# Performance work log

Hardware: AMD Instinct MI355X
Metric: run time of the kernel (lower is better)

The kernel has to match this reference:

```python
import jax, jax.numpy as jnp
import numpy as np

H = 16        # num heads
ALPHA = 1.3   # entmax alpha
N_ITER = 50   # bisection iterations
EPS = 1e-5    # layernorm eps


def entmax_bisect(x, alpha=ALPHA, n_iter=N_ITER):
    # x: (..., K). Bisection entmax along last axis (Peters et al. 2019).
    am1 = alpha - 1.0
    x = x - jnp.max(x, axis=-1, keepdims=True)
    m = jnp.max(x, axis=-1, keepdims=True)  # == 0 after shift
    lo, hi = m - 10.0, m + 10.0
    def step(carry, _):
        lo, hi = carry
        mid = 0.5 * (lo + hi)
        p = jnp.maximum(am1 * x - mid, 0.0) ** (1.0 / am1)
        gt = jnp.sum(p, axis=-1, keepdims=True) > 1.0
        return (jnp.where(gt, mid, lo), jnp.where(gt, hi, mid)), None
    (lo, hi), _ = jax.lax.scan(jax.checkpoint(step), (lo, hi), None, length=n_iter)
    p = jnp.maximum(am1 * x - hi, 0.0) ** (1.0 / am1)
    return p / (jnp.sum(p, axis=-1, keepdims=True) + 1e-12)


def _heads(t, B, N, hd):
    return t.reshape(B, N, H, hd).transpose(0, 2, 1, 3)  # (B,H,N,hd)


def attn_branch(x, mask, wq, bq, wk, bk, wv, bv, wo, bo, use_entmax):
    B, N, D = x.shape
    hd = D // H
    q = _heads(x @ wq + bq, B, N, hd)
    k = _heads(x @ wk + bk, B, N, hd)
    v = _heads(x @ wv + bv, B, N, hd)
    s = jnp.einsum('bhqd,bhkd->bhqk', q, k) / float(np.sqrt(hd)) + mask
    if use_entmax:
        s = s - jnp.max(s, axis=-1, keepdims=True)
        a = entmax_bisect(s)
    else:
        a = jax.nn.softmax(s, axis=-1)
    o = jnp.einsum('bhqk,bhkd->bhqd', a, v).transpose(0, 2, 1, 3).reshape(B, N, D)
    return o @ wo + bo


def layer_norm(x, g, b):
    m = jnp.mean(x, axis=-1, keepdims=True)
    v = jnp.mean((x - m) ** 2, axis=-1, keepdims=True)
    return (x - m) * jax.lax.rsqrt(v + EPS) * g + b


def setup_inputs():
    B, N, D, F, FILM, NMODS = 4, 512, 2048, 8192, 64, 10000
    key = jax.random.key(0)
    ks = iter(jax.random.split(key, 64))
    rn = lambda *s: jax.random.normal(next(ks), s, dtype=jnp.float32)
    inp = dict(
        x=rn(B, N, D),
        attn_mask_intra=jnp.zeros((N, N), jnp.float32),
        attn_mask_inter=jnp.zeros((N, N), jnp.float32),
        mods=jax.random.randint(next(ks), (B, N), 0, 9999),
        film_emb=rn(NMODS, FILM) * 0.02,
        film_gw=rn(FILM, D) * 0.02, film_gb=jnp.zeros((D,), jnp.float32),
        film_bw=rn(FILM, D) * 0.02, film_bb=jnp.zeros((D,), jnp.float32),
        gate_alpha=jnp.zeros((2,), jnp.float32),
        ln1_g=jnp.ones((D,), jnp.float32), ln1_b=jnp.zeros((D,), jnp.float32),
        ln2_g=jnp.ones((D,), jnp.float32), ln2_b=jnp.zeros((D,), jnp.float32),
        ffn_w1=rn(D, F) * 0.02, ffn_b1=jnp.zeros((F,), jnp.float32),
        ffn_w2=rn(F, D) * 0.02, ffn_b2=jnp.zeros((D,), jnp.float32),
    )
    for tag in ('a', 'e'):
        for nm in ('q', 'k', 'v', 'o'):
            inp['w%s_%s' % (nm, tag)] = rn(D, D) * 0.02
            inp['b%s_%s' % (nm, tag)] = jnp.zeros((D,), jnp.float32)
    return inp


def reference(x, attn_mask_intra, attn_mask_inter, mods,
              film_emb, film_gw, film_gb, film_bw, film_bb,
              gate_alpha, ln1_g, ln1_b, ln2_g, ln2_b,
              ffn_w1, ffn_b1, ffn_w2, ffn_b2,
              wq_a, bq_a, wk_a, bk_a, wv_a, bv_a, wo_a, bo_a,
              wq_e, bq_e, wk_e, bk_e, wv_e, bv_e, wo_e, bo_e):
    # FiLM modulation on the intra-module branch input
    e = film_emb[jnp.clip(mods, 1, None)]                      # (B,N,FILM)
    y_intra = (1.0 + e @ film_gw + film_gb) * x + (e @ film_bw + film_bb)
    z_intra = attn_branch(y_intra, attn_mask_intra, wq_a, bq_a, wk_a, bk_a,
                          wv_a, bv_a, wo_a, bo_a, use_entmax=False)
    z_inter = attn_branch(x, attn_mask_inter, wq_e, bq_e, wk_e, bk_e,
                          wv_e, bv_e, wo_e, bo_e, use_entmax=True)
    w = jax.nn.softmax(gate_alpha)                              # global gate
    z = w[0] * z_intra + w[1] * z_inter
    h = layer_norm(x + z, ln1_g, ln1_b)                         # Post-LN
    y = jax.nn.relu(h @ ffn_w1 + ffn_b1) @ ffn_w2 + ffn_b2
    return layer_norm(h + y, ln2_g, ln2_b)
```

## Files before the change

kernel.cpp:

```cpp
#include <hip/hip_runtime.h>
#include <hip/hip_bf16.h>

typedef float f32x4 __attribute__((ext_vector_type(4)));
typedef short bf16x8 __attribute__((ext_vector_type(8)));
typedef unsigned short u16;

#define SEQ    512
#define DIM    2048
#define NHEAD  16
#define HDIM   128
#define BATCH  4
#define BTOK   2048
#define FFDIM  8192
#define DSZ    ((long)BTOK*DIM)
#define QKVN   (3*DIM)
#define QKVSZ  ((long)BTOK*QKVN)
#define ISS    0.08838834764831845f

__device__ __forceinline__ u16 f2bf(float f){
  union{float fv;unsigned u;}c;c.fv=f;
  unsigned r=c.u+0x7FFFu+((c.u>>16)&1u); return (u16)(r>>16);
}
__device__ __forceinline__ float bf2f(u16 v){
  union{unsigned u;float f;}c;c.u=((unsigned)v)<<16;return c.f;
}
__device__ __forceinline__ float pow103(float t){
  return __builtin_amdgcn_exp2f(__builtin_amdgcn_logf(t)*(10.0f/3.0f));
}

#define GLD16(g,l) __builtin_amdgcn_global_load_lds( \
    (const __attribute__((address_space(1))) unsigned int*)(g), \
    (__attribute__((address_space(3))) unsigned int*)(l), 16, 0, 0)

#define MF(a,b,c) __builtin_amdgcn_mfma_f32_16x16x32_bf16(a,b,c,0,0,0)
#define VMW(n) do{ asm volatile("s_waitcnt vmcnt(" #n ")" ::: "memory"); \
                   __builtin_amdgcn_sched_barrier(0); }while(0)
#define LGKM0() do{ asm volatile("s_waitcnt lgkmcnt(0)" ::: "memory"); \
                    __builtin_amdgcn_sched_barrier(0); }while(0)
#define BARR() do{ asm volatile("" ::: "memory"); __builtin_amdgcn_s_barrier(); \
                   asm volatile("" ::: "memory"); }while(0)

__global__ __launch_bounds__(256, 3)
void gemm4(const u16* __restrict__ A, int lda, long sAo, long sAi,
           const u16* __restrict__ B, int ldb, long sBo, long sBi,
           void* __restrict__ C, int ldc, long sCo, int outbf,
           const float* __restrict__ bias, long sbias,
           int K, int hdiv, int relu)
{
  __shared__ __align__(16) u16 sm[24576];
  char* smb = (char*)sm;

  int gx = gridDim.x, gy = gridDim.y;
  int nwg = gx*gy*gridDim.z;
  int flat = (blockIdx.z*gy + blockIdx.y)*gx + blockIdx.x;
  int cpx = nwg >> 3; flat = (flat & 7)*cpx + (flat >> 3);
  int by = flat % gy; int tq = flat / gy; int bx = tq % gx; int bz = tq / gx;

  int zo = bz / hdiv, zi = bz - zo*hdiv;
  const u16* Ab = A + (long)zo*sAo + (long)zi*sAi;
  const u16* Bb = B + (long)zo*sBo + (long)zi*sBi;
  int m0 = by*128, n0 = bx*128;

  int tid = threadIdx.x, lane = tid & 63, w = tid >> 6;
  int wrow = (w>>1)*64, wn = (w&1)*64;
  int lr = lane & 15, lg = lane >> 4;

  int stR[2], stC[2], ldsch[2];
  #pragma unroll
  for (int q = 0; q < 2; q++) {
    int chunk = q*4 + w;
    int r = chunk*16 + (lane>>2);
    int c = (lane&3)*16;
    int Rz = r ^ ((r>>2)&1);
    int Cz = c ^ ((((r>>2)^r)&1)<<4) ^ (((r>>1)&1)<<5);
    stR[q] = Rz; stC[q] = Cz>>1;
    ldsch[q] = chunk*1024;
  }

  int aoff = ((wrow + lr)*64 + lg*16) ^ ((lane&7)<<4);
  int boff = ((wn  + lr)*64 + lg*16) ^ ((lane&7)<<4);

  f32x4 acc[4][4] = {};
  int NT = K >> 5;

  auto STG = [&](int buf, int op, int kt) {
    const u16* gp = op ? Bb : Ab;
    int ld   = op ? ldb : lda;
    int base = op ? n0 : m0;
    int kcol = kt*32;
    #pragma unroll
    for (int q = 0; q < 2; q++) {
      const u16* src = gp + (long)(base + stR[q])*ld + kcol + stC[q];
      char* dst = smb + buf*16384 + op*8192 + ldsch[q];
      GLD16(src, dst);
    }
  };

  STG(0,0,0); STG(0,1,0);
  STG(1,0,1); STG(1,1,1);

  int buf = 0;
  for (int t = 0; t < NT; t++) {
    char* Ax = smb + buf*16384;
    char* Bx = smb + buf*16384 + 8192;

    if (t+2 < NT) {
      int nb = buf + 2; if (nb >= 3) nb -= 3;
      STG(nb,0,t+2); STG(nb,1,t+2);
      VMW(8);
    } else if (t+1 < NT) { VMW(4); }
    else                 { VMW(0); }
    BARR();

    bf16x8 af[4], bv[4];
    #pragma unroll
    for (int i = 0; i < 4; i++) af[i] = *(const bf16x8*)(Ax + aoff + i*1024);
    #pragma unroll
    for (int j = 0; j < 4; j++) bv[j] = *(const bf16x8*)(Bx + boff + j*1024);
    LGKM0();
    __builtin_amdgcn_s_setprio(1);
    #pragma unroll
    for (int i = 0; i < 4; i++) {
      acc[i][0] = MF(af[i], bv[0], acc[i][0]);
      acc[i][1] = MF(af[i], bv[1], acc[i][1]);
      acc[i][2] = MF(af[i], bv[2], acc[i][2]);
      acc[i][3] = MF(af[i], bv[3], acc[i][3]);
    }
    __builtin_amdgcn_s_setprio(0);
    BARR();
    buf++; if (buf == 3) buf = 0;
  }

  if (outbf) {
    u16* Cb = (u16*)C + (long)bz*sCo;
    #pragma unroll
    for (int j = 0; j < 4; j++) {
      int col = n0 + wn + j*16 + lr;
      float bv2 = bias ? bias[zo*sbias + col] : 0.0f;
      #pragma unroll
      for (int i = 0; i < 4; i++) {
        #pragma unroll
        for (int e = 0; e < 4; e++) {
          int row = m0 + wrow + i*16 + lg*4 + e;
          float v = acc[i][j][e] + bv2;
          if (relu) v = fmaxf(v, 0.0f);
          Cb[(long)row*ldc + col] = f2bf(v);
        }
      }
    }
  } else {
    float* Cb = (float*)C + (long)bz*sCo;
    #pragma unroll
    for (int j = 0; j < 4; j++) {
      int col = n0 + wn + j*16 + lr;
      #pragma unroll
      for (int i = 0; i < 4; i++) {
        #pragma unroll
        for (int e = 0; e < 4; e++) {
          int row = m0 + wrow + i*16 + lg*4 + e;
          Cb[(long)row*ldc + col] = acc[i][j][e];
        }
      }
    }
  }
}

template<int ENTMAX>
__global__ __launch_bounds__(256, 2)
void qkprobs(const u16* __restrict__ QKVp, long brOff,
             const float* __restrict__ maskp, u16* __restrict__ P)
{
  __shared__ __align__(16) u16 sm[40960];
  char* smb = (char*)sm;

  int m0 = blockIdx.x*64;
  int z  = blockIdx.y;
  int b  = z >> 4, h = z & 15;
  const u16* Qb = QKVp + brOff + (long)b*SEQ*QKVN + h*HDIM;
  const u16* Kb = Qb + DIM;

  int tid = threadIdx.x, lane = tid & 63, w = tid >> 6;
  int lr = lane & 15, lg = lane >> 4;
  int wn = w*128;

  int rl = lane >> 2;
  int cb = (lane & 3)*16;

  int aoff = (lr*64 + lg*16) ^ ((lane&7)<<4);
  int boff = ((wn + lr)*64 + lg*16) ^ ((lane&7)<<4);

  auto stgA = [&](int kt) {
    int r = w*16 + rl;
    int Rz = r ^ ((r>>2)&1);
    int Cz = cb ^ ((((r>>2)^r)&1)<<4) ^ (((r>>1)&1)<<5);
    GLD16(Qb + (long)(m0+Rz)*QKVN + kt*32 + (Cz>>1), smb + kt*4096 + w*1024);
  };
  auto stgB = [&](int buf, int kt) {
    #pragma unroll
    for (int q = 0; q < 8; q++) {
      int chunk = q*4 + w;
      int r = chunk*16 + rl;
      int Rz = r ^ ((r>>2)&1);
      int Cz = cb ^ ((((r>>2)^r)&1)<<4) ^ (((r>>1)&1)<<5);
      GLD16(Kb + (long)Rz*QKVN + kt*32 + (Cz>>1),
            smb + 16384 + buf*32768 + chunk*1024);
    }
  };

  f32x4 acc[4][8] = {};

  stgA(0); stgA(1); stgA(2); stgA(3);
  stgB(0,0);

  #pragma unroll
  for (int kt = 0; kt < 4; kt++) {
    if (kt < 3) { stgB((kt+1)&1, kt+1); VMW(8); } else { VMW(0); }
    BARR();
    char* Bx = smb + 16384 + (kt&1)*32768;
    bf16x8 af[4], bv[8];
    #pragma unroll
    for (int i = 0; i < 4; i++) af[i] = *(const bf16x8*)(smb + kt*4096 + aoff + i*1024);
    #pragma unroll
    for (int j = 0; j < 8; j++) bv[j] = *(const bf16x8*)(Bx + boff + j*1024);
    LGKM0();
    __builtin_amdgcn_s_setprio(1);
    #pragma unroll
    for (int i = 0; i < 4; i++)
      #pragma unroll
      for (int j = 0; j < 8; j++)
        acc[i][j] = MF(af[i], bv[j], acc[i][j]);
    __builtin_amdgcn_s_setprio(0);
    BARR();
  }

  float* redA = (float*)smb;
  float* redB = (float*)(smb + 1024);

  float rmax[16];
  #pragma unroll
  for (int s = 0; s < 16; s++) rmax[s] = -3.4e38f;
  #pragma unroll
  for (int i = 0; i < 4; i++) {
    #pragma unroll
    for (int e = 0; e < 4; e++) {
      int row = i*16 + lg*4 + e;
      const float* mp = maskp + (long)(m0+row)*SEQ + wn + lr;
      #pragma unroll
      for (int j = 0; j < 8; j++) {
        float v = acc[i][j][e]*ISS + mp[j*16];
        acc[i][j][e] = v;
        rmax[i*4+e] = fmaxf(rmax[i*4+e], v);
      }
    }
  }
  #pragma unroll
  for (int s = 0; s < 16; s++)
    #pragma unroll
    for (int o = 1; o < 16; o <<= 1) rmax[s] = fmaxf(rmax[s], __shfl_xor(rmax[s], o));
  if (lr == 0) {
    #pragma unroll
    for (int i = 0; i < 4; i++)
      #pragma unroll
      for (int e = 0; e < 4; e++) redA[w*64 + i*16 + lg*4 + e] = rmax[i*4+e];
  }
  BARR();
  #pragma unroll
  for (int i = 0; i < 4; i++)
    #pragma unroll
    for (int e = 0; e < 4; e++) {
      int row = i*16 + lg*4 + e;
      rmax[i*4+e] = fmaxf(fmaxf(redA[row], redA[64+row]),
                          fmaxf(redA[128+row], redA[192+row]));
    }
  BARR();

  float inv[16];

  if (ENTMAX) {
    #pragma unroll
    for (int i = 0; i < 4; i++)
      #pragma unroll
      for (int j = 0; j < 8; j++)
        #pragma unroll
        for (int e = 0; e < 4; e++)
          acc[i][j][e] = (acc[i][j][e] - rmax[i*4+e])*0.3f;

    float lo[16], hi[16], tau[16];
    #pragma unroll
    for (int s = 0; s < 16; s++) { lo[s] = -1.0f; hi[s] = 0.0f; }

    #pragma unroll 1
    for (int it = 0; it < 5; it++) {
      float ps[16];
      #pragma unroll
      for (int s = 0; s < 16; s++) ps[s] = 0.0f;
      #pragma unroll
      for (int i = 0; i < 4; i++)
        #pragma unroll
        for (int e = 0; e < 4; e++) {
          float mid = 0.5f*(lo[i*4+e] + hi[i*4+e]);
          #pragma unroll
          for (int j = 0; j < 8; j++) {
            float t = acc[i][j][e] - mid;
            if (t > 0.0f) ps[i*4+e] += pow103(t);
          }
        }
      #pragma unroll
      for (int s = 0; s < 16; s++)
        #pragma unroll
        for (int o = 1; o < 16; o <<= 1) ps[s] += __shfl_xor(ps[s], o);
      if (lr == 0) {
        #pragma unroll
        for (int i = 0; i < 4; i++)
          #pragma unroll
          for (int e = 0; e < 4; e++) redA[w*64 + i*16 + lg*4 + e] = ps[i*4+e];
      }
      BARR();
      #pragma unroll
      for (int i = 0; i < 4; i++)
        #pragma unroll
        for (int e = 0; e < 4; e++) {
          int row = i*16 + lg*4 + e, s = i*4+e;
          float tot = redA[row] + redA[64+row] + redA[128+row] + redA[192+row];
          float mid = 0.5f*(lo[s] + hi[s]);
          bool gt = tot > 1.0f;
          lo[s] = gt ? mid : lo[s];
          hi[s] = gt ? hi[s] : mid;
        }
      BARR();
    }
    #pragma unroll
    for (int s = 0; s < 16; s++) tau[s] = 0.5f*(lo[s] + hi[s]);

    #pragma unroll 1
    for (int it = 0; it < 5; it++) {
      float ps[16], pd[16];
      #pragma unroll
      for (int s = 0; s < 16; s++) { ps[s] = 0.0f; pd[s] = 0.0f; }
      #pragma unroll
      for (int i = 0; i < 4; i++)
        #pragma unroll
        for (int e = 0; e < 4; e++) {
          float tv = tau[i*4+e];
          #pragma unroll
          for (int j = 0; j < 8; j++) {
            float t = acc[i][j][e] - tv;
            if (t > 0.0f) {
              float w7 = __builtin_amdgcn_exp2f(__builtin_amdgcn_logf(t)*(7.0f/3.0f));
              pd[i*4+e] += w7; ps[i*4+e] += w7*t;
            }
          }
        }
      #pragma unroll
      for (int s = 0; s < 16; s++)
        #pragma unroll
        for (int o = 1; o < 16; o <<= 1) {
          ps[s] += __shfl_xor(ps[s], o);
          pd[s] += __shfl_xor(pd[s], o);
        }
      if (lr == 0) {
        #pragma unroll
        for (int i = 0; i < 4; i++)
          #pragma unroll
          for (int e = 0; e < 4; e++) {
            redA[w*64 + i*16 + lg*4 + e] = ps[i*4+e];
            redB[w*64 + i*16 + lg*4 + e] = pd[i*4+e];
          }
      }
      BARR();
      #pragma unroll
      for (int i = 0; i < 4; i++)
        #pragma unroll
        for (int e = 0; e < 4; e++) {
          int row = i*16 + lg*4 + e, s = i*4+e;
          float st = redA[row] + redA[64+row] + redA[128+row] + redA[192+row];
          float dt = redB[row] + redB[64+row] + redB[128+row] + redB[192+row];
          bool gt = st > 1.0f;
          lo[s] = gt ? tau[s] : lo[s];
          hi[s] = gt ? hi[s] : tau[s];
          float tn = tau[s] + (st - 1.0f) / ((10.0f/3.0f)*dt + 1e-30f);
          tau[s] = (tn > lo[s] && tn < hi[s]) ? tn : 0.5f*(lo[s] + hi[s]);
        }
      BARR();
    }

    float ps[16];
    #pragma unroll
    for (int s = 0; s < 16; s++) ps[s] = 0.0f;
    #pragma unroll
    for (int i = 0; i < 4; i++)
      #pragma unroll
      for (int e = 0; e < 4; e++) {
        float tv = tau[i*4+e];
        #pragma unroll
        for (int j = 0; j < 8; j++) {
          float t = acc[i][j][e] - tv;
          float p = (t > 0.0f) ? pow103(t) : 0.0f;
          acc[i][j][e] = p;
          ps[i*4+e] += p;
        }
      }
    #pragma unroll
    for (int s = 0; s < 16; s++)
      #pragma unroll
      for (int o = 1; o < 16; o <<= 1) ps[s] += __shfl_xor(ps[s], o);
    if (lr == 0) {
      #pragma unroll
      for (int i = 0; i < 4; i++)
        #pragma unroll
        for (int e = 0; e < 4; e++) redA[w*64 + i*16 + lg*4 + e] = ps[i*4+e];
    }
    BARR();
    #pragma unroll
    for (int i = 0; i < 4; i++)
      #pragma unroll
      for (int e = 0; e < 4; e++) {
        int row = i*16 + lg*4 + e;
        inv[i*4+e] = 1.0f/(redA[row] + redA[64+row] + redA[128+row] + redA[192+row] + 1e-12f);
      }
  } else {
    float ps[16];
    #pragma unroll
    for (int s = 0; s < 16; s++) ps[s] = 0.0f;
    #pragma unroll
    for (int i = 0; i < 4; i++)
      #pragma unroll
      for (int e = 0; e < 4; e++) {
        float mx = rmax[i*4+e];
        #pragma unroll
        for (int j = 0; j < 8; j++) {
          float p = __expf(acc[i][j][e] - mx);
          acc[i][j][e] = p;
          ps[i*4+e] += p;
        }
      }
    #pragma unroll
    for (int s = 0; s < 16; s++)
      #pragma unroll
      for (int o = 1; o < 16; o <<= 1) ps[s] += __shfl_xor(ps[s], o);
    if (lr == 0) {
      #pragma unroll
      for (int i = 0; i < 4; i++)
        #pragma unroll
        for (int e = 0; e < 4; e++) redA[w*64 + i*16 + lg*4 + e] = ps[i*4+e];
    }
    BARR();
    #pragma unroll
    for (int i = 0; i < 4; i++)
      #pragma unroll
      for (int e = 0; e < 4; e++) {
        int row = i*16 + lg*4 + e;
        inv[i*4+e] = 1.0f/(redA[row] + redA[64+row] + redA[128+row] + redA[192+row]);
      }
  }

  u16* Pb = P + ((long)z*SEQ + m0)*SEQ;
  #pragma unroll
  for (int i = 0; i < 4; i++)
    #pragma unroll
    for (int e = 0; e < 4; e++) {
      int row = i*16 + lg*4 + e;
      u16* pr = Pb + (long)row*SEQ + wn + lr;
      #pragma unroll
      for (int j = 0; j < 8; j++)
        pr[j*16] = f2bf(acc[i][j][e]*inv[i*4+e]);
    }
}

__global__ __launch_bounds__(256)
void redk(const float* __restrict__ Pp, int nk, const float* __restrict__ bias,
          u16* __restrict__ out)
{
  long i = ((long)blockIdx.x*256 + threadIdx.x)*8;
  long z = i >> 22;
  int  n = (int)(i & 2047);
  float v[8] = {};
  for (int k = 0; k < nk; k++) {
    const float* s = Pp + (z*nk + k)*DSZ + (i & (DSZ-1));
    f32x4 aa = *(const f32x4*)s, bb = *(const f32x4*)(s+4);
    v[0]+=aa.x; v[1]+=aa.y; v[2]+=aa.z; v[3]+=aa.w;
    v[4]+=bb.x; v[5]+=bb.y; v[6]+=bb.z; v[7]+=bb.w;
  }
  f32x4 b0 = *(const f32x4*)&bias[z*2048 + n], b1 = *(const f32x4*)&bias[z*2048 + n + 4];
  float bv[8] = {b0.x,b0.y,b0.z,b0.w,b1.x,b1.y,b1.z,b1.w};
  u16 w[8] __attribute__((aligned(16)));
  #pragma unroll
  for (int j = 0; j < 8; j++) w[j] = f2bf(v[j] + bv[j]);
  *(bf16x8*)&out[i] = *(bf16x8*)w;
}

template<int BN_, int WM_, int WN_>
__global__ __launch_bounds__(256)
void gemm_lds(const u16* __restrict__ A, int lda, long sAo, long sAi,
              const u16* __restrict__ B, int ldb, long sBo, long sBi,
              void* __restrict__ C, int ldc, long sCo, long sCi, int outbf,
              const float* __restrict__ bias, long sbias,
              float alpha, int K, int hdiv, int relu)
{
  constexpr int BM_ = 128;
  constexpr int MI = BM_/WM_/16;
  constexpr int NJ = BN_/WN_/16;
  __shared__ __align__(16) u16 As[BM_*32];
  __shared__ __align__(16) u16 Bs[BN_*32];

  int z = blockIdx.z, zo = z/hdiv, zi = z - zo*hdiv;
  const u16* Ab = A + zo*sAo + zi*sAi;
  const u16* Bb = B + zo*sBo + zi*sBi;

  int m0 = blockIdx.y*BM_, n0 = blockIdx.x*BN_;
  int tid = threadIdx.x, lane = tid & 63, wid = tid >> 6;
  int wrow = (wid/WN_)*(BM_/WM_), wcol = (wid%WN_)*(BN_/WN_);
  int lr = lane & 15, lg = lane >> 4;
  int srow = lane >> 2, skc = (lane & 3)*8;

  f32x4 acc[MI][NJ] = {};

  for (int k0 = 0; k0 < K; k0 += 32) {
    #pragma unroll
    for (int e = 0; e < BM_/64; e++) {
      int c = wid*(BM_/64) + e, row = c*16 + srow;
      GLD16(Ab + (long)(m0 + row)*lda + k0 + skc, &As[c*512]);
    }
    #pragma unroll
    for (int e = 0; e < BN_/64; e++) {
      int c = wid*(BN_/64) + e, row = c*16 + srow;
      GLD16(Bb + (long)(n0 + row)*ldb + k0 + skc, &Bs[c*512]);
    }
    __syncthreads();
    bf16x8 af[MI], bfv[NJ];
    #pragma unroll
    for (int i = 0; i < MI; i++)
      af[i] = *(const bf16x8*)&As[(wrow + i*16 + lr)*32 + lg*8];
    #pragma unroll
    for (int j = 0; j < NJ; j++)
      bfv[j] = *(const bf16x8*)&Bs[(wcol + j*16 + lr)*32 + lg*8];
    #pragma unroll
    for (int i = 0; i < MI; i++)
      #pragma unroll
      for (int j = 0; j < NJ; j++)
        acc[i][j] = MF(af[i], bfv[j], acc[i][j]);
    __syncthreads();
  }

  long coff = zo*sCo + zi*sCi;
  #pragma unroll
  for (int j = 0; j < NJ; j++) {
    int col = n0 + wcol + j*16 + lr;
    float bv = bias ? bias[zo*sbias + col] : 0.0f;
    #pragma unroll
    for (int i = 0; i < MI; i++) {
      #pragma unroll
      for (int e = 0; e < 4; e++) {
        int row = m0 + wrow + i*16 + lg*4 + e;
        float v = alpha*acc[i][j][e] + bv;
        if (relu)  v = fmaxf(v, 0.0f);
        long idx = coff + (long)row*ldc + col;
        if (outbf) ((u16*)C)[idx] = f2bf(v);
        else       ((float*)C)[idx] = v;
      }
    }
  }
}

__global__ __launch_bounds__(256)
void wtrans(const float* __restrict__ W, int ldw, u16* __restrict__ Wt, int ldt)
{
  __shared__ u16 t[64][72];
  int tid = threadIdx.x, r = tid >> 2, c0 = (tid & 3)*16;
  long gr = (long)blockIdx.y*64 + r, gc = (long)blockIdx.x*64 + c0;
  #pragma unroll
  for (int u = 0; u < 16; u += 4) {
    f32x4 v = *(const f32x4*)&W[gr*ldw + gc + u];
    t[r][c0+u+0]=f2bf(v.x); t[r][c0+u+1]=f2bf(v.y);
    t[r][c0+u+2]=f2bf(v.z); t[r][c0+u+3]=f2bf(v.w);
  }
  __syncthreads();
  u16 o[16] __attribute__((aligned(16)));
  #pragma unroll
  for (int u = 0; u < 16; u++) o[u] = t[c0+u][r];
  u16* dst = &Wt[(long)(blockIdx.x*64 + r)*ldt + blockIdx.y*64 + c0];
  *(bf16x8*)&dst[0] = *(bf16x8*)&o[0];
  *(bf16x8*)&dst[8] = *(bf16x8*)&o[8];
}

__global__ __launch_bounds__(256)
void vtrans(const u16* __restrict__ V, u16* __restrict__ Vt)
{
  __shared__ u16 t[64][72];
  int z = blockIdx.z, b = z >> 4, h = z & 15;
  const u16* src = V + (long)b*SEQ*QKVN + h*HDIM;
  u16* dst = Vt + (long)z*HDIM*SEQ;
  int tid = threadIdx.x, r = tid >> 2, c0 = (tid & 3)*16;
  int tok0 = blockIdx.x*64, d0 = blockIdx.y*64;
  #pragma unroll
  for (int u = 0; u < 16; u += 8) {
    bf16x8 v = *(const bf16x8*)&src[(long)(tok0+r)*QKVN + d0 + c0 + u];
    #pragma unroll
    for (int e = 0; e < 8; e++) t[r][c0+u+e] = (u16)v[e];
  }
  __syncthreads();
  u16 o[16] __attribute__((aligned(16)));
  #pragma unroll
  for (int u = 0; u < 16; u++) o[u] = t[c0+u][r];
  *(bf16x8*)&dst[(long)(d0+r)*SEQ + tok0 + c0]     = *(bf16x8*)&o[0];
  *(bf16x8*)&dst[(long)(d0+r)*SEQ + tok0 + c0 + 8] = *(bf16x8*)&o[8];
}

__global__ __launch_bounds__(256)
void f32_to_bf16(const float* __restrict__ in, u16* __restrict__ o, long n8)
{
  long i = (long)blockIdx.x*256 + threadIdx.x;
  if (i >= n8) return; i *= 8;
  f32x4 a = *(const f32x4*)&in[i], b = *(const f32x4*)&in[i+4];
  u16 w[8] __attribute__((aligned(16)));
  w[0]=f2bf(a.x);w[1]=f2bf(a.y);w[2]=f2bf(a.z);w[3]=f2bf(a.w);
  w[4]=f2bf(b.x);w[5]=f2bf(b.y);w[6]=f2bf(b.z);w[7]=f2bf(b.w);
  *(bf16x8*)&o[i] = *(bf16x8*)w;
}

__global__ __launch_bounds__(256)
void egather(const int* __restrict__ mods, const float* __restrict__ emb, u16* __restrict__ E)
{
  int i = blockIdx.x*256 + threadIdx.x;
  int row = i >> 3, j0 = (i & 7)*8;
  int m = mods[row]; if (m < 1) m = 1;
  const float* s = &emb[(long)m*64 + j0];
  f32x4 a = *(const f32x4*)s, b = *(const f32x4*)(s+4);
  u16 w[8] __attribute__((aligned(16)));
  w[0]=f2bf(a.x);w[1]=f2bf(a.y);w[2]=f2bf(a.z);w[3]=f2bf(a.w);
  w[4]=f2bf(b.x);w[5]=f2bf(b.y);w[6]=f2bf(b.z);w[7]=f2bf(b.w);
  *(bf16x8*)&E[(long)row*64 + j0] = *(bf16x8*)w;
}

__global__ __launch_bounds__(256)
void film_apply(const float* __restrict__ x, const u16* __restrict__ G,
                const u16* __restrict__ B, u16* __restrict__ y)
{
  long i = ((long)blockIdx.x*256 + threadIdx.x)*8;
  f32x4 x0 = *(const f32x4*)&x[i], x1 = *(const f32x4*)&x[i+4];
  bf16x8 g = *(const bf16x8*)&G[i], b = *(const bf16x8*)&B[i];
  float xv[8] = {x0.x,x0.y,x0.z,x0.w,x1.x,x1.y,x1.z,x1.w};
  u16 w[8] __attribute__((aligned(16)));
  #pragma unroll
  for (int e = 0; e < 8; e++)
    w[e] = f2bf((1.0f + bf2f((u16)g[e]))*xv[e] + bf2f((u16)b[e]));
  *(bf16x8*)&y[i] = *(bf16x8*)w;
}

__global__ __launch_bounds__(256)
void pack_bias(float* __restrict__ dst,
               const float* q_a, const float* k_a, const float* v_a,
               const float* q_e, const float* k_e, const float* v_e,
               const float* o_a, const float* o_e,
               const float* fg, const float* fb)
{
  int i = blockIdx.x*256 + threadIdx.x;
  if (i < 12288) {
    int br = i/6144, r = i - br*6144, sel = r >> 11, o = r & 2047;
    const float* s = br ? (sel==0?q_e:sel==1?k_e:v_e)
                        : (sel==0?q_a:sel==1?k_a:v_a);
    dst[i] = s[o];
  } else if (i < 16384) {
    int r = i - 12288; dst[i] = (r>>11) ? o_e[r&2047] : o_a[r&2047];
  } else {
    int r = i - 16384; dst[i] = (r>>11) ? fb[r&2047] : fg[r&2047];
  }
}

__global__ __launch_bounds__(256)
void ln_gate(const float* __restrict__ x, const u16* __restrict__ z0,
             const u16* __restrict__ z1, const float* __restrict__ ga,
             const float* __restrict__ g, const float* __restrict__ b,
             u16* __restrict__ h)
{
  __shared__ float red[8];
  long base = (long)blockIdx.x*DIM;
  int t8 = threadIdx.x*8, lane = threadIdx.x & 63, wid = threadIdx.x >> 6;
  float a0 = ga[0], a1 = ga[1];
  float mm = fmaxf(a0,a1), e0 = __expf(a0-mm), e1 = __expf(a1-mm);
  float w0 = e0/(e0+e1), w1 = e1/(e0+e1);
  f32x4 x0 = *(const f32x4*)&x[base+t8], x1 = *(const f32x4*)&x[base+t8+4];
  bf16x8 zi = *(const bf16x8*)&z0[base+t8], ze = *(const bf16x8*)&z1[base+t8];
  float xv[8] = {x0.x,x0.y,x0.z,x0.w,x1.x,x1.y,x1.z,x1.w};
  float v[8]; float s = 0.0f;
  #pragma unroll
  for (int j = 0; j < 8; j++) {
    v[j] = xv[j] + w0*bf2f((u16)zi[j]) + w1*bf2f((u16)ze[j]);
    s += v[j];
  }
  for (int o = 32; o; o >>= 1) s += __shfl_xor(s, o);
  if (lane == 0) red[wid] = s;
  __syncthreads();
  float mean = (red[0]+red[1]+red[2]+red[3])*(1.0f/DIM);
  float q = 0.0f;
  #pragma unroll
  for (int j = 0; j < 8; j++) { float d = v[j]-mean; q += d*d; }
  for (int o = 32; o; o >>= 1) q += __shfl_xor(q, o);
  if (lane == 0) red[4+wid] = q;
  __syncthreads();
  float inv = rsqrtf((red[4]+red[5]+red[6]+red[7])*(1.0f/DIM) + 1e-5f);
  f32x4 g0 = *(const f32x4*)&g[t8], g1 = *(const f32x4*)&g[t8+4];
  f32x4 b0 = *(const f32x4*)&b[t8], b1 = *(const f32x4*)&b[t8+4];
  float gv[8] = {g0.x,g0.y,g0.z,g0.w,g1.x,g1.y,g1.z,g1.w};
  float bv[8] = {b0.x,b0.y,b0.z,b0.w,b1.x,b1.y,b1.z,b1.w};
  u16 w[8] __attribute__((aligned(16)));
  #pragma unroll
  for (int j = 0; j < 8; j++) w[j] = f2bf((v[j]-mean)*inv*gv[j] + bv[j]);
  *(bf16x8*)&h[base+t8] = *(bf16x8*)w;
}

__global__ __launch_bounds__(256)
void ln_res(const u16* __restrict__ hin, const u16* __restrict__ y,
            const float* __restrict__ g, const float* __restrict__ b,
            float* __restrict__ out)
{
  __shared__ float red[8];
  long base = (long)blockIdx.x*DIM;
  int t8 = threadIdx.x*8, lane = threadIdx.x & 63, wid = threadIdx.x >> 6;
  bf16x8 hv = *(const bf16x8*)&hin[base+t8], yv = *(const bf16x8*)&y[base+t8];
  float v[8]; float s = 0.0f;
  #pragma unroll
  for (int j = 0; j < 8; j++) { v[j] = bf2f((u16)hv[j]) + bf2f((u16)yv[j]); s += v[j]; }
  for (int o = 32; o; o >>= 1) s += __shfl_xor(s, o);
  if (lane == 0) red[wid] = s;
  __syncthreads();
  float mean = (red[0]+red[1]+red[2]+red[3])*(1.0f/DIM);
  float q = 0.0f;
  #pragma unroll
  for (int j = 0; j < 8; j++) { float d = v[j]-mean; q += d*d; }
  for (int o = 32; o; o >>= 1) q += __shfl_xor(q, o);
  if (lane == 0) red[4+wid] = q;
  __syncthreads();
  float inv = rsqrtf((red[4]+red[5]+red[6]+red[7])*(1.0f/DIM) + 1e-5f);
  f32x4 g0 = *(const f32x4*)&g[t8], g1 = *(const f32x4*)&g[t8+4];
  f32x4 b0 = *(const f32x4*)&b[t8], b1 = *(const f32x4*)&b[t8+4];
  float gv[8] = {g0.x,g0.y,g0.z,g0.w,g1.x,g1.y,g1.z,g1.w};
  float bv[8] = {b0.x,b0.y,b0.z,b0.w,b1.x,b1.y,b1.z,b1.w};
  f32x4 o0, o1;
  #pragma unroll
  for (int j = 0; j < 4; j++) o0[j] = (v[j]-mean)*inv*gv[j] + bv[j];
  #pragma unroll
  for (int j = 0; j < 4; j++) o1[j] = (v[4+j]-mean)*inv*gv[4+j] + bv[4+j];
  *(f32x4*)&out[base+t8] = o0;
  *(f32x4*)&out[base+t8+4] = o1;
}

static void G128(hipStream_t st, const u16* A,int lda,long sAo,long sAi,
                 const u16* B,int ldb,long sBo,long sBi,
                 void* C,int ldc,long sCo,long sCi,int outbf,
                 const float* bias,long sbias,
                 float alpha,int M,int N,int K,int batch,int hdiv,int relu)
{
  gemm_lds<128,2,2><<<dim3(N/128,M/128,batch),dim3(256),0,st>>>(
      A,lda,sAo,sAi,B,ldb,sBo,sBi,C,ldc,sCo,sCi,outbf,bias,sbias,alpha,K,hdiv,relu);
}
static void G64(hipStream_t st, const u16* A,int lda,long sAo,long sAi,
                const u16* B,int ldb,long sBo,long sBi,
                void* C,int ldc,long sCo,long sCi,int outbf,
                const float* bias,long sbias,
                float alpha,int M,int N,int K,int batch,int hdiv,int relu)
{
  gemm_lds<64,4,1><<<dim3(N/64,M/128,batch),dim3(256),0,st>>>(
      A,lda,sAo,sAi,B,ldb,sBo,sBi,C,ldc,sCo,sCi,outbf,bias,sbias,alpha,K,hdiv,relu);
}
static void G4(hipStream_t st, const u16* A,int lda,long sAo,long sAi,
               const u16* B,int ldb,long sBo,long sBi,
               void* C,int ldc,long sCo,int outbf,
               const float* bias,long sbias,int M,int N,int K,int batch,int hdiv,int relu)
{
  gemm4<<<dim3(N/128,M/128,batch),dim3(256),0,st>>>(
      A,lda,sAo,sAi,B,ldb,sBo,sBi,C,ldc,sCo,outbf,bias,sbias,K,hdiv,relu);
}

extern "C" void kernel_launch(void* const* d_in, const int* in_sizes, int n_in,
                              void* d_out, int out_size, void* d_ws, size_t ws_size,
                              hipStream_t stream)
{
  const float* x          = (const float*)d_in[0];
  const float* mask_intra = (const float*)d_in[1];
  const float* mask_inter = (const float*)d_in[2];
  const int*   mods       = (const int*)  d_in[3];
  const float* film_emb   = (const float*)d_in[4];
  const float* film_gw    = (const float*)d_in[5];
  const float* film_gb    = (const float*)d_in[6];
  const float* film_bw    = (const float*)d_in[7];
  const float* film_bb    = (const float*)d_in[8];
  const float* gate_alpha = (const float*)d_in[9];
  const float* ln1_g = (const float*)d_in[10];
  const float* ln1_b = (const float*)d_in[11];
  const float* ln2_g = (const float*)d_in[12];
  const float* ln2_b = (const float*)d_in[13];
  const float* ffn_w1 = (const float*)d_in[14];
  const float* ffn_b1 = (const float*)d_in[15];
  const float* ffn_w2 = (const float*)d_in[16];
  const float* ffn_b2 = (const float*)d_in[17];
  const float* wq_a = (const float*)d_in[18]; const float* bq_a = (const float*)d_in[19];
  const float* wk_a = (const float*)d_in[20]; const float* bk_a = (const float*)d_in[21];
  const float* wv_a = (const float*)d_in[22]; const float* bv_a = (const float*)d_in[23];
  const float* wo_a = (const float*)d_in[24]; const float* bo_a = (const float*)d_in[25];
  const float* wq_e = (const float*)d_in[26]; const float* bq_e = (const float*)d_in[27];
  const float* wk_e = (const float*)d_in[28]; const float* bk_e = (const float*)d_in[29];
  const float* wv_e = (const float*)d_in[30]; const float* bv_e = (const float*)d_in[31];
  const float* wo_e = (const float*)d_in[32]; const float* bo_e = (const float*)d_in[33];

  char* ws = (char*)d_ws;
  u16*   ybf  = (u16*)(ws);
  u16*   xbf  = (u16*)(ws + (8L<<20));
  u16*   QKV  = (u16*)(ws + (16L<<20));
  u16*   Gf   = QKV;
  u16*   Bfm  = QKV + DSZ;
  u16*   zbuf = (u16*)(ws + (16L<<20));
  u16*   hbf  = (u16*)(ws + (32L<<20));
  u16*   Wst  = (u16*)(ws + (64L<<20));
  u16*   mid  = (u16*)(ws + (96L<<20));
  u16*   P    = (u16*)(ws + (128L<<20));
  float* Pf2  = (float*)(ws + (128L<<20));
  u16*   f2o  = (u16*)(ws);
  u16*   Vt   = (u16*)(ws + (160L<<20));
  u16*   Ebuf = (u16*)(ws + (160L<<20));
  u16*   Wfm  = (u16*)(ws + (161L<<20));
  u16*   AO   = (u16*)(ws + (168L<<20));
  float* bpk  = (float*)(ws + (184L<<20));

  f32_to_bf16<<<2048,256,0,stream>>>(x, xbf, DSZ/8);
  egather<<<64,256,0,stream>>>(mods, film_emb, Ebuf);
  wtrans<<<dim3(32,1),256,0,stream>>>(film_gw, DIM, Wfm, 64);
  wtrans<<<dim3(32,1),256,0,stream>>>(film_bw, DIM, Wfm + (long)DIM*64, 64);
  pack_bias<<<80,256,0,stream>>>(bpk, bq_a,bk_a,bv_a, bq_e,bk_e,bv_e, bo_a,bo_e, film_gb,film_bb);

  G128(stream, Ebuf,64,0,0, Wfm,64,(long)DIM*64,0, Gf,DIM,DSZ,0,1,
       bpk+16384,2048, 1.0f, BTOK,DIM,64, 2,1,0);
  film_apply<<<2048,256,0,stream>>>(x, Gf, Bfm, ybf);

  const float* wsrc[6] = {wq_a,wk_a,wv_a, wq_e,wk_e,wv_e};
  for (int i = 0; i < 6; i++)
    wtrans<<<dim3(32,32),256,0,stream>>>(wsrc[i], DIM, Wst + (long)i*DIM*DIM, DIM);
  G4(stream, ybf,DIM,DSZ,0, Wst,DIM,(long)QKVN*DIM,0, QKV,QKVN,QKVSZ,1,
     bpk,QKVN, BTOK,QKVN,DIM, 2,1, 0);

  for (int br = 0; br < 2; br++) {
    long brOff = (long)br*QKVSZ;
    const u16* Vb = QKV + brOff + 2*DIM;
    if (br == 0)
      qkprobs<0><<<dim3(8,64),dim3(256),0,stream>>>(QKV, brOff, mask_intra, P);
    else
      qkprobs<1><<<dim3(8,64),dim3(256),0,stream>>>(QKV, brOff, mask_inter, P);
    vtrans<<<dim3(8,2,64),256,0,stream>>>(Vb, Vt);
    G64(stream, P,SEQ,(long)NHEAD*SEQ*SEQ,(long)SEQ*SEQ,
        Vt,SEQ,(long)NHEAD*HDIM*SEQ,(long)HDIM*SEQ,
        AO + (long)br*DSZ,DIM,(long)SEQ*DIM,HDIM,1, nullptr,0,
        1.0f, SEQ,HDIM,SEQ, BATCH*NHEAD,NHEAD,0);
  }

  wtrans<<<dim3(32,32),256,0,stream>>>(wo_a, DIM, Wst, DIM);
  wtrans<<<dim3(32,32),256,0,stream>>>(wo_e, DIM, Wst + (long)DIM*DIM, DIM);
  G4(stream, AO,DIM,DSZ,0, Wst,DIM,(long)DIM*DIM,0, zbuf,DIM,DSZ,1,
     bpk+12288,DIM, BTOK,DIM,DIM, 2,1, 0);

  ln_gate<<<2048,256,0,stream>>>(x, zbuf, zbuf+DSZ, gate_alpha, ln1_g, ln1_b, hbf);

  wtrans<<<dim3(128,32),256,0,stream>>>(ffn_w1, FFDIM, Wst, DIM);
  G4(stream, hbf,DIM,0,0, Wst,DIM,0,0, mid,FFDIM,0,1,
     ffn_b1,0, BTOK,FFDIM,DIM, 1,1, 1);
  wtrans<<<dim3(32,128),256,0,stream>>>(ffn_w2, DIM, Wst, FFDIM);
  G4(stream, mid,FFDIM,4096,0, Wst,FFDIM,4096,0, Pf2,DIM,DSZ,0,
     nullptr,0, BTOK,DIM,4096, 2,1, 0);
  redk<<<2048,256,0,stream>>>(Pf2, 2, ffn_b2, f2o);

  ln_res<<<2048,256,0,stream>>>(hbf, f2o, ln2_g, ln2_b, (float*)d_out);
}
```

Measured before the change: 665.7 us.

## Add 128x256-tile GEMM for QKV and FFN1, batch weight transposes

Adds a wider 128x256 output-tile GEMM kernel with triple-buffered LDS staging and uses it for the QKV projection and the FFN up-projection. Each wave now computes 128x64, which raises MFMA work per LDS load and cuts A-tile reloads. The cost is more LDS and registers per block (occupancy hint drops to 2). It also merges the separate per-weight transpose launches into one batched launch indexed by blockIdx.z, which removes launch overhead.

```diff
diff --git a/kernel.cpp b/kernel.cpp
--- a/kernel.cpp
+++ b/kernel.cpp
@@ -40,6 +40,116 @@
 #define BARR() do{ asm volatile("" ::: "memory"); __builtin_amdgcn_s_barrier(); \
                    asm volatile("" ::: "memory"); }while(0)
 
+__global__ __launch_bounds__(256, 2)
+void gemm4w(const u16* __restrict__ A, int lda, long sAo, long sAi,
+            const u16* __restrict__ B, int ldb, long sBo, long sBi,
+            u16* __restrict__ C, int ldc, long sCo,
+            const float* __restrict__ bias, long sbias,
+            int K, int hdiv, int relu)
+{
+  __shared__ __align__(16) u16 sm[36864];
+  char* smb = (char*)sm;
+
+  int gx = gridDim.x, gy = gridDim.y;
+  int nwg = gx*gy*gridDim.z;
+  int flat = (blockIdx.z*gy + blockIdx.y)*gx + blockIdx.x;
+  int cpx = nwg >> 3; flat = (flat & 7)*cpx + (flat >> 3);
+  int by = flat % gy; int tq = flat / gy; int bx = tq % gx; int bz = tq / gx;
+
+  int zo = bz / hdiv, zi = bz - zo*hdiv;
+  const u16* Ab = A + (long)zo*sAo + (long)zi*sAi;
+  const u16* Bb = B + (long)zo*sBo + (long)zi*sBi;
+  int m0 = by*128, n0 = bx*256;
+
+  int tid = threadIdx.x, lane = tid & 63, w = tid >> 6;
+  int lr = lane & 15, lg = lane >> 4;
+  int rl = lane >> 2, cbyte = (lane & 3)*16;
+
+  int sRA[2], sCA[2];
+  #pragma unroll
+  for (int q = 0; q < 2; q++) {
+    int r = (2*w+q)*16 + rl;
+    sRA[q] = r ^ ((r>>2)&1);
+    sCA[q] = (cbyte ^ ((((r>>2)^r)&1)<<4) ^ (((r>>1)&1)<<5)) >> 1;
+  }
+  int sRB[4], sCB[4];
+  #pragma unroll
+  for (int q = 0; q < 4; q++) {
+    int r = (4*w+q)*16 + rl;
+    sRB[q] = r ^ ((r>>2)&1);
+    sCB[q] = (cbyte ^ ((((r>>2)^r)&1)<<4) ^ (((r>>1)&1)<<5)) >> 1;
+  }
+
+  int aoff = (lr*64 + lg*16) ^ ((lane&7)<<4);
+  int boff = w*4096 + ((lr*64 + lg*16) ^ ((lane&7)<<4));
+
+  f32x4 acc[8][4] = {};
+  int NT = K >> 5;
+
+  auto STG = [&](int buf, int kt) {
+    int kcol = kt*32;
+    char* base = smb + buf*24576;
+    #pragma unroll
+    for (int q = 0; q < 2; q++)
+      GLD16(Ab + (long)(m0 + sRA[q])*lda + kcol + sCA[q], base + (2*w+q)*1024);
+    #pragma unroll
+    for (int q = 0; q < 4; q++)
+      GLD16(Bb + (long)(n0 + sRB[q])*ldb + kcol + sCB[q], base + 8192 + (4*w+q)*1024);
+  };
+
+  STG(0,0);
+  if (NT > 1) STG(1,1);
+
+  int buf = 0;
+  for (int t = 0; t < NT; t++) {
+    char* Ax = smb + buf*24576;
+    char* Bx = Ax + 8192;
+
+    if (t+2 < NT) {
+      int nb = buf + 2; if (nb >= 3) nb -= 3;
+      STG(nb, t+2);
+      VMW(12);
+    } else if (t+1 < NT) { VMW(6); }
+    else                 { VMW(0); }
+    BARR();
+
+    bf16x8 af[8], bv[4];
+    #pragma unroll
+    for (int i = 0; i < 8; i++) af[i] = *(const bf16x8*)(Ax + aoff + i*1024);
+    #pragma unroll
+    for (int j = 0; j < 4; j++) bv[j] = *(const bf16x8*)(Bx + boff + j*1024);
+    LGKM0();
+    __builtin_amdgcn_s_setprio(1);
+    #pragma unroll
+    for (int i = 0; i < 8; i++) {
+      acc[i][0] = MF(af[i], bv[0], acc[i][0]);
+      acc[i][1] = MF(af[i], bv[1], acc[i][1]);
+      acc[i][2] = MF(af[i], bv[2], acc[i][2]);
+      acc[i][3] = MF(af[i], bv[3], acc[i][3]);
+    }
+    __builtin_amdgcn_s_setprio(0);
+    BARR();
+    buf++; if (buf == 3) buf = 0;
+  }
+
+  u16* Cb = C + (long)bz*sCo;
+  #pragma unroll
+  for (int j = 0; j < 4; j++) {
+    int col = n0 + w*64 + j*16 + lr;
+    float bv2 = bias ? bias[zo*sbias + col] : 0.0f;
+    #pragma unroll
+    for (int i = 0; i < 8; i++) {
+      #pragma unroll
+      for (int e = 0; e < 4; e++) {
+        int row = m0 + i*16 + lg*4 + e;
+        float v = acc[i][j][e] + bv2;
+        if (relu) v = fmaxf(v, 0.0f);
+        Cb[(long)row*ldc + col] = f2bf(v);
+      }
+    }
+  }
+}
+
 __global__ __launch_bounds__(256, 3)
 void gemm4(const u16* __restrict__ A, int lda, long sAo, long sAi,
            const u16* __restrict__ B, int ldb, long sBo, long sBi,
@@ -562,6 +672,31 @@
   }
 }
 
+struct P6 { const float* p[6]; };
+
+__global__ __launch_bounds__(256)
+void wtrans6(P6 srcs, int ldw, u16* __restrict__ Wt, long dstStride, int ldt)
+{
+  __shared__ u16 t[64][72];
+  const float* W = srcs.p[blockIdx.z];
+  u16* Wd = Wt + (long)blockIdx.z*dstStride;
+  int tid = threadIdx.x, r = tid >> 2, c0 = (tid & 3)*16;
+  long gr = (long)blockIdx.y*64 + r, gc = (long)blockIdx.x*64 + c0;
+  #pragma unroll
+  for (int u = 0; u < 16; u += 4) {
+    f32x4 v = *(const f32x4*)&W[gr*ldw + gc + u];
+    t[r][c0+u+0]=f2bf(v.x); t[r][c0+u+1]=f2bf(v.y);
+    t[r][c0+u+2]=f2bf(v.z); t[r][c0+u+3]=f2bf(v.w);
+  }
+  __syncthreads();
+  u16 o[16] __attribute__((aligned(16)));
+  #pragma unroll
+  for (int u = 0; u < 16; u++) o[u] = t[c0+u][r];
+  u16* dst = &Wd[(long)(blockIdx.x*64 + r)*ldt + blockIdx.y*64 + c0];
+  *(bf16x8*)&dst[0] = *(bf16x8*)&o[0];
+  *(bf16x8*)&dst[8] = *(bf16x8*)&o[8];
+}
+
 __global__ __launch_bounds__(256)
 void wtrans(const float* __restrict__ W, int ldw, u16* __restrict__ Wt, int ldt)
 {
@@ -770,6 +905,14 @@
 {
   gemm4<<<dim3(N/128,M/128,batch),dim3(256),0,st>>>(
       A,lda,sAo,sAi,B,ldb,sBo,sBi,C,ldc,sCo,outbf,bias,sbias,K,hdiv,relu);
+}
+static void G4W(hipStream_t st, const u16* A,int lda,long sAo,long sAi,
+                const u16* B,int ldb,long sBo,long sBi,
+                u16* C,int ldc,long sCo,
+                const float* bias,long sbias,int M,int N,int K,int batch,int hdiv,int relu)
+{
+  gemm4w<<<dim3(N/256,M/128,batch),dim3(256),0,st>>>(
+      A,lda,sAo,sAi,B,ldb,sBo,sBi,C,ldc,sCo,bias,sbias,K,hdiv,relu);
 }
 
 extern "C" void kernel_launch(void* const* d_in, const int* in_sizes, int n_in,
@@ -824,19 +967,24 @@
 
   f32_to_bf16<<<2048,256,0,stream>>>(x, xbf, DSZ/8);
   egather<<<64,256,0,stream>>>(mods, film_emb, Ebuf);
-  wtrans<<<dim3(32,1),256,0,stream>>>(film_gw, DIM, Wfm, 64);
-  wtrans<<<dim3(32,1),256,0,stream>>>(film_bw, DIM, Wfm + (long)DIM*64, 64);
+  {
+    P6 pf; pf.p[0]=film_gw; pf.p[1]=film_bw;
+    pf.p[2]=film_gw; pf.p[3]=film_gw; pf.p[4]=film_gw; pf.p[5]=film_gw;
+    wtrans6<<<dim3(32,1,2),256,0,stream>>>(pf, DIM, Wfm, (long)DIM*64, 64);
+  }
   pack_bias<<<80,256,0,stream>>>(bpk, bq_a,bk_a,bv_a, bq_e,bk_e,bv_e, bo_a,bo_e, film_gb,film_bb);
 
   G128(stream, Ebuf,64,0,0, Wfm,64,(long)DIM*64,0, Gf,DIM,DSZ,0,1,
        bpk+16384,2048, 1.0f, BTOK,DIM,64, 2,1,0);
   film_apply<<<2048,256,0,stream>>>(x, Gf, Bfm, ybf);
 
-  const float* wsrc[6] = {wq_a,wk_a,wv_a, wq_e,wk_e,wv_e};
-  for (int i = 0; i < 6; i++)
-    wtrans<<<dim3(32,32),256,0,stream>>>(wsrc[i], DIM, Wst + (long)i*DIM*DIM, DIM);
-  G4(stream, ybf,DIM,DSZ,0, Wst,DIM,(long)QKVN*DIM,0, QKV,QKVN,QKVSZ,1,
-     bpk,QKVN, BTOK,QKVN,DIM, 2,1, 0);
+  {
+    P6 pq; pq.p[0]=wq_a; pq.p[1]=wk_a; pq.p[2]=wv_a;
+    pq.p[3]=wq_e; pq.p[4]=wk_e; pq.p[5]=wv_e;
+    wtrans6<<<dim3(32,32,6),256,0,stream>>>(pq, DIM, Wst, (long)DIM*DIM, DIM);
+  }
+  G4W(stream, ybf,DIM,DSZ,0, Wst,DIM,(long)QKVN*DIM,0, QKV,QKVN,QKVSZ,
+      bpk,QKVN, BTOK,QKVN,DIM, 2,1, 0);
 
   for (int br = 0; br < 2; br++) {
     long brOff = (long)br*QKVSZ;
@@ -852,16 +1000,19 @@
         1.0f, SEQ,HDIM,SEQ, BATCH*NHEAD,NHEAD,0);
   }
 
-  wtrans<<<dim3(32,32),256,0,stream>>>(wo_a, DIM, Wst, DIM);
-  wtrans<<<dim3(32,32),256,0,stream>>>(wo_e, DIM, Wst + (long)DIM*DIM, DIM);
+  {
+    P6 po; po.p[0]=wo_a; po.p[1]=wo_e;
+    po.p[2]=wo_a; po.p[3]=wo_a; po.p[4]=wo_a; po.p[5]=wo_a;
+    wtrans6<<<dim3(32,32,2),256,0,stream>>>(po, DIM, Wst, (long)DIM*DIM, DIM);
+  }
   G4(stream, AO,DIM,DSZ,0, Wst,DIM,(long)DIM*DIM,0, zbuf,DIM,DSZ,1,
      bpk+12288,DIM, BTOK,DIM,DIM, 2,1, 0);
 
   ln_gate<<<2048,256,0,stream>>>(x, zbuf, zbuf+DSZ, gate_alpha, ln1_g, ln1_b, hbf);
 
   wtrans<<<dim3(128,32),256,0,stream>>>(ffn_w1, FFDIM, Wst, DIM);
-  G4(stream, hbf,DIM,0,0, Wst,DIM,0,0, mid,FFDIM,0,1,
-     ffn_b1,0, BTOK,FFDIM,DIM, 1,1, 1);
+  G4W(stream, hbf,DIM,0,0, Wst,DIM,0,0, mid,FFDIM,0,
+      ffn_b1,0, BTOK,FFDIM,DIM, 1,1, 1);
   wtrans<<<dim3(32,128),256,0,stream>>>(ffn_w2, DIM, Wst, FFDIM);
   G4(stream, mid,FFDIM,4096,0, Wst,FFDIM,4096,0, Pf2,DIM,DSZ,0,
      nullptr,0, BTOK,DIM,4096, 2,1, 0);
```

New measurement: 623.9 us. 6.3% less time.
